# Performance work log

Hardware: AMD Instinct MI355X
Metric: run time of the kernel (lower is better)

## Reference

```python
import jax, jax.numpy as jnp
import numpy as np

HIDDEN = 2048
NUM_HEADS = 16
HEAD_DIM = HIDDEN // NUM_HEADS  # 128
ROPE_BASE = 10000.0


def setup_inputs() -> dict:
    key = jax.random.key(0)
    ks = jax.random.split(key, 5)
    B, T, C = 2, 2048, HIDDEN
    scale = 1.0 / np.sqrt(C)
    x = jax.random.normal(ks[0], (B, T, C), dtype=jnp.float32)
    Wq = jax.random.normal(ks[1], (C, C), dtype=jnp.float32) * scale
    Wk = jax.random.normal(ks[2], (C, C), dtype=jnp.float32) * scale
    Wv = jax.random.normal(ks[3], (C, C), dtype=jnp.float32) * scale
    Wo = jax.random.normal(ks[4], (C, C), dtype=jnp.float32) * scale
    return {"x": x, "Wq": Wq, "Wk": Wk, "Wv": Wv, "Wo": Wo}


def _rope_cos_sin(T, dtype):
    # inv_freq: [D/2]; emb: [T, D] = cat(freqs, freqs)
    inv_freq = 1.0 / (ROPE_BASE ** (jnp.arange(0, HEAD_DIM, 2, dtype=jnp.float32) / HEAD_DIM))
    t = jnp.arange(T, dtype=jnp.float32)
    freqs = t[:, None] * inv_freq[None, :]          # [T, D/2]
    emb = jnp.concatenate([freqs, freqs], axis=-1)  # [T, D]
    # broadcast shape [1, T, 1, D] to match q/k [B, T, H, D]
    return jnp.cos(emb)[None, :, None, :].astype(dtype), jnp.sin(emb)[None, :, None, :].astype(dtype)


def _rotate_half(u):
    u1, u2 = jnp.split(u, 2, axis=-1)
    return jnp.concatenate([-u2, u1], axis=-1)


def reference(x, Wq, Wk, Wv, Wo):
    B, T, C = x.shape
    H, D = NUM_HEADS, HEAD_DIM
    # QKV projections (torch Linear: x @ W.T). Weights here stored as [C, C] so use x @ W.
    q = (x @ Wq).reshape(B, T, H, D)
    k = (x @ Wk).reshape(B, T, H, D)
    v = (x @ Wv).reshape(B, T, H, D)
    cos, sin = _rope_cos_sin(T, x.dtype)
    q = q * cos + _rotate_half(q) * sin
    k = k * cos + _rotate_half(k) * sin
    # causal SDPA: scores [B, H, T, T]
    scale = 1.0 / jnp.sqrt(jnp.asarray(D, dtype=x.dtype))
    scores = jnp.einsum('bqhd,bkhd->bhqk', q, k) * scale
    causal = jnp.tril(jnp.ones((T, T), dtype=bool))
    scores = jnp.where(causal[None, None, :, :], scores, jnp.asarray(-jnp.inf, dtype=scores.dtype))
    attn = jax.nn.softmax(scores, axis=-1)
    out = jnp.einsum('bhqk,bkhd->bqhd', attn, v).reshape(B, T, C)
    return out @ Wo
```

## Files before the change

kernel.cpp:

```cpp
#include <hip/hip_runtime.h>
#include <hip/hip_bf16.h>

#define C_DIM 2048
#define NHEAD 16
#define HD 128
#define BB 2
#define TT 2048
#define MM (BB * TT)
#define NQT 32
#define N3 (3 * C_DIM)

typedef short short4v __attribute__((ext_vector_type(4)));
typedef short short8v __attribute__((ext_vector_type(8)));
typedef __bf16 bf16x4 __attribute__((ext_vector_type(4)));
typedef __bf16 bf16x8 __attribute__((ext_vector_type(8)));
typedef float f32x4 __attribute__((ext_vector_type(4)));

#define AS1 __attribute__((address_space(1)))
#define AS3 __attribute__((address_space(3)))

#define VMCNT(n) asm volatile("s_waitcnt vmcnt(" #n ")" ::: "memory")

__device__ __forceinline__ void load_lds16(const void* g, void* l) {
  __builtin_amdgcn_global_load_lds((const AS1 void*)g, (AS3 void*)l, 16, 0, 0);
}

__device__ __forceinline__ short f2bf(float f) {
  union { float f; unsigned u; } v; v.f = f;
  unsigned u = v.u;
  u += 0x7FFFu + ((u >> 16) & 1u);
  return (short)(u >> 16);
}
__device__ __forceinline__ float bf2f(short s) {
  union { unsigned u; float f; } v;
  v.u = ((unsigned)(unsigned short)s) << 16;
  return v.f;
}

__device__ __forceinline__ float exp2_fast(float x) {
  float r;
  asm("v_exp_f32 %0, %1" : "=v"(r) : "v"(x));
  return r;
}

__global__ __launch_bounds__(256) void cvt_x(const float* __restrict__ in,
                                             short* __restrict__ out, int n4) {
  int i = blockIdx.x * 256 + threadIdx.x;
  int stride = gridDim.x * 256;
  for (int idx = i; idx < n4; idx += stride) {
    float4 f = ((const float4*)in)[idx];
    short4v o;
    o[0] = f2bf(f.x); o[1] = f2bf(f.y); o[2] = f2bf(f.z); o[3] = f2bf(f.w);
    ((short4v*)out)[idx] = o;
  }
}

__global__ __launch_bounds__(256) void cvt_w_all(const float* __restrict__ Wq,
                                                 const float* __restrict__ Wk,
                                                 const float* __restrict__ Wv,
                                                 const float* __restrict__ Wo,
                                                 short* __restrict__ Wt) {
  __shared__ float tile[32][33];
  int z = blockIdx.z;
  const float* W = z == 0 ? Wq : z == 1 ? Wk : z == 2 ? Wv : Wo;
  short* dst = Wt + (size_t)z * C_DIM * C_DIM;
  int bx = blockIdx.x;
  int by = blockIdx.y;
  int lx = threadIdx.x & 31;
  int ly = threadIdx.x >> 5;
#pragma unroll
  for (int j = 0; j < 4; ++j) {
    int r = by * 32 + ly + j * 8;
    tile[ly + j * 8][lx] = W[(size_t)r * C_DIM + bx * 32 + lx];
  }
  __syncthreads();
#pragma unroll
  for (int j = 0; j < 4; ++j) {
    int n = bx * 32 + ly + j * 8;
    dst[(size_t)n * C_DIM + by * 32 + lx] = f2bf(tile[lx][ly + j * 8]);
  }
}

__global__ __launch_bounds__(256) void rope_tab(float2* __restrict__ tab) {
  int idx = blockIdx.x * 256 + threadIdx.x;
  int t = idx >> 6, d = idx & 63;
  float inv = expf(-9.210340371976184f * (float)d * (1.0f / 64.0f));
  float a = (float)t * inv;
  tab[idx] = make_float2(cosf(a), sinf(a));
}

template <bool F32OUT>
__global__ __launch_bounds__(512, 4) void gemm8w(const short* __restrict__ A,
                                                 const short* __restrict__ Bt,
                                                 void* __restrict__ Cout,
                                                 int M, int N, int K, int NBN) {
  __shared__ short sA[2][128 * 64];
  __shared__ short sB[2][128 * 64];
  const int tid = threadIdx.x;
  const int lane = tid & 63;
  const int w = tid >> 6;
  const int wm = w >> 2, wn = w & 3;
  const int r = lane & 15, g = lane >> 4;

  const int wg = blockIdx.x;
  const int mb = wg / NBN, nb = wg % NBN;
  const int m0 = mb * 128, n0 = nb * 128;

  f32x4 acc[4][2] = {};

  auto stage = [&](int buf, int kt) {
#pragma unroll
    for (int j = 0; j < 2; ++j) {
      int p = j * 512 + tid;
      int row = p >> 3;
      int c16 = (p & 7) ^ (row & 7);
      load_lds16(A + (size_t)(m0 + row) * K + kt * 64 + c16 * 8,
                 &sA[buf][(j * 512 + w * 64) * 8]);
    }
#pragma unroll
    for (int j = 0; j < 2; ++j) {
      int p = j * 512 + tid;
      int row = p >> 3;
      int c16 = (p & 7) ^ (row & 7);
      load_lds16(Bt + (size_t)(n0 + row) * K + kt * 64 + c16 * 8,
                 &sB[buf][(j * 512 + w * 64) * 8]);
    }
  };

  auto compute = [&](int buf) {
#pragma unroll
    for (int kk = 0; kk < 2; ++kk) {
      bf16x8 af[4], bv[2];
#pragma unroll
      for (int m = 0; m < 4; ++m) {
        int row = wm * 64 + m * 16 + r;
        af[m] = *(const bf16x8*)((const char*)&sA[buf][0] + row * 128 +
                                 (((kk * 4 + g) ^ (row & 7)) << 4));
      }
#pragma unroll
      for (int n = 0; n < 2; ++n) {
        int row = wn * 32 + n * 16 + r;
        bv[n] = *(const bf16x8*)((const char*)&sB[buf][0] + row * 128 +
                                 (((kk * 4 + g) ^ (row & 7)) << 4));
      }
      __builtin_amdgcn_s_setprio(1);
#pragma unroll
      for (int m = 0; m < 4; ++m)
#pragma unroll
        for (int n = 0; n < 2; ++n)
          acc[m][n] = __builtin_amdgcn_mfma_f32_16x16x32_bf16(af[m], bv[n], acc[m][n], 0, 0, 0);
      __builtin_amdgcn_s_setprio(0);
    }
  };

  const int NT = K >> 6;
  stage(0, 0);
  stage(1, 1);
  VMCNT(4);
  __builtin_amdgcn_s_barrier();

  for (int t = 0; t < NT; ++t) {
    const int cur = t & 1;
    compute(cur);
    if (t + 1 < NT) {
      asm volatile("" ::: "memory");
      __builtin_amdgcn_s_barrier();
      if (t + 2 < NT) {
        stage(cur, t + 2);
        VMCNT(4);
      } else {
        VMCNT(0);
      }
      asm volatile("" ::: "memory");
      __builtin_amdgcn_s_barrier();
    }
  }

#pragma unroll
  for (int m = 0; m < 4; ++m)
#pragma unroll
    for (int n = 0; n < 2; ++n)
#pragma unroll
      for (int q = 0; q < 4; ++q) {
        int row = m0 + wm * 64 + m * 16 + g * 4 + q;
        int col = n0 + wn * 32 + n * 16 + r;
        size_t off = (size_t)row * N + col;
        if constexpr (F32OUT) ((float*)Cout)[off] = acc[m][n][q];
        else ((short*)Cout)[off] = f2bf(acc[m][n][q]);
      }
}

__global__ __launch_bounds__(256) void rope_qk(const short* __restrict__ qkv,
                                               const float2* __restrict__ tab,
                                               short* __restrict__ Qr,
                                               short* __restrict__ Kr) {
  const short* src = qkv + (blockIdx.y ? C_DIM : 0);
  short* dst = blockIdx.y ? Kr : Qr;
  const float qs = blockIdx.y ? 1.0f : 0.12751744f;
  int rid = blockIdx.x * 4 + (threadIdx.x >> 6);
  int lane = threadIdx.x & 63;
  int t = rid & (TT - 1);
  int bh = rid >> 11;
  int b = bh >> 4, h = bh & 15;
  const short* in = src + ((size_t)(b * TT + t)) * N3 + h * HD;

  int v = *(const int*)(in + 2 * lane);
  int pv = __shfl_xor(v, 32, 64);
  float f0 = bf2f((short)(v & 0xFFFF)),  f1 = bf2f((short)(v >> 16));
  float p0 = bf2f((short)(pv & 0xFFFF)), p1 = bf2f((short)(pv >> 16));
  float4 cst = *(const float4*)(tab + (size_t)t * 64 + ((2 * lane) & 63));
  float s = (lane < 32) ? -1.0f : 1.0f;
  float o0 = (f0 * cst.x + s * p0 * cst.y) * qs;
  float o1 = (f1 * cst.z + s * p1 * cst.w) * qs;
  unsigned out2 = ((unsigned)(unsigned short)f2bf(o0)) |
                  (((unsigned)(unsigned short)f2bf(o1)) << 16);
  *(unsigned*)(dst + (size_t)rid * HD + 2 * lane) = out2;
}

__global__ __launch_bounds__(256) void v_tr(const short* __restrict__ qkv,
                                            short* __restrict__ Vt) {
  __shared__ short tl[64][132];
  int bh = blockIdx.y, b = bh >> 4, h = bh & 15;
  int t0 = blockIdx.x * 64;
  int tid = threadIdx.x;
  const short* vsrc = qkv + 2 * C_DIM;
#pragma unroll
  for (int i = 0; i < 4; ++i) {
    int c = i * 256 + tid;
    int row = c >> 4, cc = c & 15;
    short8v v = *(const short8v*)(vsrc + ((size_t)(b * TT + t0 + row)) * N3 + h * HD + cc * 8);
#pragma unroll
    for (int j = 0; j < 8; ++j) tl[row][cc * 8 + j] = v[j];
  }
  __syncthreads();
  int d = tid >> 1, half = tid & 1;
#pragma unroll
  for (int u = 0; u < 4; ++u) {
    short8v ov;
#pragma unroll
    for (int j = 0; j < 8; ++j) ov[j] = tl[half * 32 + u * 8 + j][d];
    *(short8v*)(Vt + ((size_t)bh * HD + d) * TT + t0 + half * 32 + u * 8) = ov;
  }
}

__global__ __launch_bounds__(256, 3) void attn_one(const short* __restrict__ Qr,
                                                   const short* __restrict__ Kr,
                                                   const short* __restrict__ Vt,
                                                   short* __restrict__ AO) {
  const int bx = blockIdx.x;
  const int j = bx >> 5, bh = bx & 31;
  const int qt = (j & 1) ? (j >> 1) : (NQT - 1 - (j >> 1));
  const int b = bh >> 4, h = bh & 15;
  const int tid = threadIdx.x;
  const int lane = tid & 63;
  const int w = tid >> 6;
  const int r = lane & 15, g = lane >> 4;

  __shared__ short sK[64 * 128];
  __shared__ short sV[128 * 64];
  __shared__ short sP[4][16 * 64];

  bf16x8 qf[4];
  {
    const short* qbp = Qr + ((size_t)bh * TT + qt * 64 + w * 16 + r) * HD + g * 8;
#pragma unroll
    for (int s = 0; s < 4; ++s) qf[s] = *(const bf16x8*)(qbp + s * 32);
  }

  f32x4 o[8] = {};
  float m = -1e30f, l = 0.f;

  short8v kreg[4], vreg[4];
  auto stage_load = [&](int kt) {
#pragma unroll
    for (int i = 0; i < 4; ++i) {
      int c = i * 256 + tid;
      kreg[i] = *(const short8v*)(Kr + ((size_t)bh * TT + kt * 64 + (c >> 4)) * HD + (c & 15) * 8);
    }
#pragma unroll
    for (int i = 0; i < 4; ++i) {
      int c = i * 256 + tid;
      vreg[i] = *(const short8v*)(Vt + ((size_t)bh * HD + (c >> 3)) * TT + kt * 64 + (c & 7) * 8);
    }
  };
  auto stage_write = [&]() {
#pragma unroll
    for (int i = 0; i < 4; ++i) {
      int c = i * 256 + tid;
      int row = c >> 4, cc = c & 15;
      int addr = (row * 256 + cc * 16) ^ ((row & 7) << 4);
      *(short8v*)((char*)sK + addr) = kreg[i];
    }
#pragma unroll
    for (int i = 0; i < 4; ++i) {
      int c = i * 256 + tid;
      int row = c >> 3, cc = c & 7;
      int addr = (row * 128 + cc * 16) ^ ((row & 7) << 4);
      *(short8v*)((char*)sV + addr) = vreg[i];
    }
  };

  char* pw = (char*)&sP[w][0];

  stage_load(0);
  stage_write();
  __syncthreads();

  for (int kt = 0; kt <= qt; ++kt) {
    f32x4 sacc[4] = {};
    __builtin_amdgcn_s_setprio(1);
#pragma unroll
    for (int nf = 0; nf < 4; ++nf) {
#pragma unroll
      for (int ss = 0; ss < 4; ++ss) {
        int krow = nf * 16 + r;
        int addr = (krow * 256 + (ss * 32 + g * 8) * 2) ^ ((krow & 7) << 4);
        bf16x8 kf = *(const bf16x8*)((char*)sK + addr);
        sacc[nf] = __builtin_amdgcn_mfma_f32_16x16x32_bf16(kf, qf[ss], sacc[nf], 0, 0, 0);
      }
    }
    __builtin_amdgcn_s_setprio(0);

    if (kt < qt) stage_load(kt + 1);

    if (kt == qt) {
#pragma unroll
      for (int nf = 0; nf < 4; ++nf)
#pragma unroll
        for (int q = 0; q < 4; ++q)
          if (nf * 16 + g * 4 + q > w * 16 + r) sacc[nf][q] = -1e30f;
    }

    float p01 = fmaxf(fmaxf(sacc[0][0], sacc[0][1]), fmaxf(sacc[0][2], sacc[0][3]));
    float p23 = fmaxf(fmaxf(sacc[1][0], sacc[1][1]), fmaxf(sacc[1][2], sacc[1][3]));
    float p45 = fmaxf(fmaxf(sacc[2][0], sacc[2][1]), fmaxf(sacc[2][2], sacc[2][3]));
    float p67 = fmaxf(fmaxf(sacc[3][0], sacc[3][1]), fmaxf(sacc[3][2], sacc[3][3]));
    float pmax = fmaxf(fmaxf(p01, p23), fmaxf(p45, p67));
    pmax = fmaxf(pmax, __shfl_xor(pmax, 16, 64));
    pmax = fmaxf(pmax, __shfl_xor(pmax, 32, 64));

    if (!__all(pmax - m <= 8.0f)) {
      float mnew = fmaxf(m, pmax);
      float alpha = exp2_fast(m - mnew);
      m = mnew;
      l *= alpha;
#pragma unroll
      for (int q = 0; q < 4; ++q) {
        float aq = __shfl(alpha, (g * 4 + q) | (lane & 48), 64);
#pragma unroll
        for (int nf2 = 0; nf2 < 8; ++nf2) o[nf2][q] *= aq;
      }
    }

    float s16 = 0.f;
#pragma unroll
    for (int nf = 0; nf < 4; ++nf) {
      f32x4 pe;
#pragma unroll
      for (int q = 0; q < 4; ++q) pe[q] = exp2_fast(sacc[nf][q] - m);
      s16 += (pe[0] + pe[1]) + (pe[2] + pe[3]);
      int addr = (r * 128 + nf * 32 + g * 8) ^ ((r & 7) << 4);
      *(bf16x4*)(pw + addr) = __builtin_convertvector(pe, bf16x4);
    }
    float rs = s16;
    rs += __shfl_xor(rs, 16, 64);
    rs += __shfl_xor(rs, 32, 64);
    l += rs;

    __builtin_amdgcn_s_setprio(1);
#pragma unroll
    for (int s2 = 0; s2 < 2; ++s2) {
      int paddr = (r * 128 + s2 * 64 + g * 16) ^ ((r & 7) << 4);
      bf16x8 pa = *(const bf16x8*)(pw + paddr);
#pragma unroll
      for (int nf2 = 0; nf2 < 8; ++nf2) {
        int drow = nf2 * 16 + r;
        int addr = (drow * 128 + (s2 * 32 + g * 8) * 2) ^ ((drow & 7) << 4);
        bf16x8 vb = *(const bf16x8*)((char*)sV + addr);
        o[nf2] = __builtin_amdgcn_mfma_f32_16x16x32_bf16(pa, vb, o[nf2], 0, 0, 0);
      }
    }
    __builtin_amdgcn_s_setprio(0);

    __syncthreads();
    if (kt < qt) {
      stage_write();
      __syncthreads();
    }
  }

  float linv = 1.0f / l;
  float lrow[4];
#pragma unroll
  for (int q = 0; q < 4; ++q)
    lrow[q] = __shfl(linv, (g * 4 + q) | (lane & 48), 64);
  short* ow = sK + w * 16 * 128;
#pragma unroll
  for (int nf2 = 0; nf2 < 8; ++nf2)
#pragma unroll
    for (int q = 0; q < 4; ++q)
      ow[(g * 4 + q) * 128 + nf2 * 16 + r] = f2bf(o[nf2][q] * lrow[q]);
  __syncthreads();

#pragma unroll
  for (int ch = 0; ch < 4; ++ch) {
    int c = ch * 256 + tid;
    int orow = c >> 4;
    int ocol = (c & 15) * 8;
    int t = qt * 64 + orow;
    *(short8v*)(AO + ((size_t)b * TT + t) * C_DIM + h * HD + ocol) =
        *(const short8v*)(sK + orow * 128 + ocol);
  }
}

extern "C" void kernel_launch(void* const* d_in, const int* in_sizes, int n_in,
                              void* d_out, int out_size, void* d_ws, size_t ws_size,
                              hipStream_t stream) {
  const float* x  = (const float*)d_in[0];
  const float* Wq = (const float*)d_in[1];
  const float* Wk = (const float*)d_in[2];
  const float* Wv = (const float*)d_in[3];
  const float* Wo = (const float*)d_in[4];

  char* ws = (char*)d_ws;
  size_t off = 0;
  auto take = [&](size_t bytes) {
    char* p = ws + off;
    off += (bytes + 255) & ~(size_t)255;
    return p;
  };
  const size_t xe = (size_t)MM * C_DIM;
  const size_t we = (size_t)C_DIM * C_DIM;
  short* xb   = (short*)take(xe * 2);
  short* wqkv = (short*)take(4 * we * 2);
  short* wot  = wqkv + 3 * we;
  short* qkv  = (short*)take(3 * xe * 2);
  short* Qr   = (short*)take(xe * 2);
  short* Kr   = (short*)take(xe * 2);
  short* Vtr  = (short*)take(xe * 2);
  float2* tab = (float2*)take((size_t)TT * 64 * sizeof(float2));
  short* AO   = qkv;

  cvt_x<<<2048, 256, 0, stream>>>(x, xb, (int)(xe / 4));
  cvt_w_all<<<dim3(64, 64, 4), 256, 0, stream>>>(Wq, Wk, Wv, Wo, wqkv);
  rope_tab<<<(TT * 64) / 256, 256, 0, stream>>>(tab);

  gemm8w<false><<<1536, 512, 0, stream>>>(xb, wqkv, qkv, MM, N3, C_DIM, N3 / 128);

  rope_qk<<<dim3(16384, 2), 256, 0, stream>>>(qkv, tab, Qr, Kr);
  v_tr<<<dim3(32, 32), 256, 0, stream>>>(qkv, Vtr);

  attn_one<<<1024, 256, 0, stream>>>(Qr, Kr, Vtr, AO);

  gemm8w<true><<<512, 512, 0, stream>>>(AO, wot, d_out, MM, C_DIM, C_DIM, C_DIM / 128);
}
```

Before: 289.4 us.

## Fuse RoPE and V transpose into QKV GEMM epilogue via LDS staging

The QKV projection GEMM now stages its 128x128 output tile in shared memory and writes Q and K directly with RoPE (and the Q scale) applied, and V directly in transposed layout. This removes the rope_qk and v_tr kernels and the round trip of the full bf16 qkv intermediate through global memory, along with two launches. In exchange the GEMM epilogue gets longer and does per-element table loads and LDS reads, which may add register pressure or bank conflicts in the epilogue.

```diff
diff --git a/kernel.cpp b/kernel.cpp
--- a/kernel.cpp
+++ b/kernel.cpp
@@ -89,13 +89,18 @@
   tab[idx] = make_float2(cosf(a), sinf(a));
 }
 
-template <bool F32OUT>
+template <int EPI>
 __global__ __launch_bounds__(512, 4) void gemm8w(const short* __restrict__ A,
                                                  const short* __restrict__ Bt,
                                                  void* __restrict__ Cout,
-                                                 int M, int N, int K, int NBN) {
-  __shared__ short sA[2][128 * 64];
-  __shared__ short sB[2][128 * 64];
+                                                 int M, int N, int K, int NBN,
+                                                 const float2* __restrict__ tab,
+                                                 short* __restrict__ Qr,
+                                                 short* __restrict__ Kr,
+                                                 short* __restrict__ Vt) {
+  __shared__ short smem[4 * 128 * 64];
+  short (*sA)[128 * 64] = (short(*)[128 * 64])smem;
+  short (*sB)[128 * 64] = (short(*)[128 * 64])(smem + 2 * 128 * 64);
   const int tid = threadIdx.x;
   const int lane = tid & 63;
   const int w = tid >> 6;
@@ -176,70 +181,72 @@
     }
   }
 
-#pragma unroll
-  for (int m = 0; m < 4; ++m)
-#pragma unroll
-    for (int n = 0; n < 2; ++n)
-#pragma unroll
-      for (int q = 0; q < 4; ++q) {
-        int row = m0 + wm * 64 + m * 16 + g * 4 + q;
-        int col = n0 + wn * 32 + n * 16 + r;
-        size_t off = (size_t)row * N + col;
-        if constexpr (F32OUT) ((float*)Cout)[off] = acc[m][n][q];
-        else ((short*)Cout)[off] = f2bf(acc[m][n][q]);
-      }
-}
-
-__global__ __launch_bounds__(256) void rope_qk(const short* __restrict__ qkv,
-                                               const float2* __restrict__ tab,
-                                               short* __restrict__ Qr,
-                                               short* __restrict__ Kr) {
-  const short* src = qkv + (blockIdx.y ? C_DIM : 0);
-  short* dst = blockIdx.y ? Kr : Qr;
-  const float qs = blockIdx.y ? 1.0f : 0.12751744f;
-  int rid = blockIdx.x * 4 + (threadIdx.x >> 6);
-  int lane = threadIdx.x & 63;
-  int t = rid & (TT - 1);
-  int bh = rid >> 11;
-  int b = bh >> 4, h = bh & 15;
-  const short* in = src + ((size_t)(b * TT + t)) * N3 + h * HD;
-
-  int v = *(const int*)(in + 2 * lane);
-  int pv = __shfl_xor(v, 32, 64);
-  float f0 = bf2f((short)(v & 0xFFFF)),  f1 = bf2f((short)(v >> 16));
-  float p0 = bf2f((short)(pv & 0xFFFF)), p1 = bf2f((short)(pv >> 16));
-  float4 cst = *(const float4*)(tab + (size_t)t * 64 + ((2 * lane) & 63));
-  float s = (lane < 32) ? -1.0f : 1.0f;
-  float o0 = (f0 * cst.x + s * p0 * cst.y) * qs;
-  float o1 = (f1 * cst.z + s * p1 * cst.w) * qs;
-  unsigned out2 = ((unsigned)(unsigned short)f2bf(o0)) |
-                  (((unsigned)(unsigned short)f2bf(o1)) << 16);
-  *(unsigned*)(dst + (size_t)rid * HD + 2 * lane) = out2;
-}
-
-__global__ __launch_bounds__(256) void v_tr(const short* __restrict__ qkv,
-                                            short* __restrict__ Vt) {
-  __shared__ short tl[64][132];
-  int bh = blockIdx.y, b = bh >> 4, h = bh & 15;
-  int t0 = blockIdx.x * 64;
-  int tid = threadIdx.x;
-  const short* vsrc = qkv + 2 * C_DIM;
-#pragma unroll
-  for (int i = 0; i < 4; ++i) {
-    int c = i * 256 + tid;
-    int row = c >> 4, cc = c & 15;
-    short8v v = *(const short8v*)(vsrc + ((size_t)(b * TT + t0 + row)) * N3 + h * HD + cc * 8);
-#pragma unroll
-    for (int j = 0; j < 8; ++j) tl[row][cc * 8 + j] = v[j];
-  }
-  __syncthreads();
-  int d = tid >> 1, half = tid & 1;
-#pragma unroll
-  for (int u = 0; u < 4; ++u) {
-    short8v ov;
-#pragma unroll
-    for (int j = 0; j < 8; ++j) ov[j] = tl[half * 32 + u * 8 + j][d];
-    *(short8v*)(Vt + ((size_t)bh * HD + d) * TT + t0 + half * 32 + u * 8) = ov;
+  if constexpr (EPI == 1) {
+#pragma unroll
+    for (int m = 0; m < 4; ++m)
+#pragma unroll
+      for (int n = 0; n < 2; ++n)
+#pragma unroll
+        for (int q = 0; q < 4; ++q) {
+          int row = m0 + wm * 64 + m * 16 + g * 4 + q;
+          int col = n0 + wn * 32 + n * 16 + r;
+          ((float*)Cout)[(size_t)row * N + col] = acc[m][n][q];
+        }
+  } else {
+    __syncthreads();
+    short* S = smem;
+#pragma unroll
+    for (int m = 0; m < 4; ++m)
+#pragma unroll
+      for (int n = 0; n < 2; ++n)
+#pragma unroll
+        for (int q = 0; q < 4; ++q) {
+          int row = wm * 64 + m * 16 + g * 4 + q;
+          int col = wn * 32 + n * 16 + r;
+          S[row * 130 + col] = f2bf(acc[m][n][q]);
+        }
+    __syncthreads();
+
+    const int z = nb >> 4;
+    const int h = nb & 15;
+    const int b = m0 >> 11;
+    const int bh = b * NHEAD + h;
+    const int t_base = m0 & (TT - 1);
+
+    if (z < 2) {
+      short* dst = (z == 0) ? Qr : Kr;
+      const float qs = (z == 0) ? 0.12751744f : 1.0f;
+#pragma unroll
+      for (int i = 0; i < 4; ++i) {
+        int c = i * 512 + tid;
+        int row = c >> 4;
+        int d0 = (c & 15) * 8;
+        int t = t_base + row;
+        bool hi = d0 >= 64;
+        int dbase = d0 & 63;
+        short8v ov;
+#pragma unroll
+        for (int jj = 0; jj < 8; ++jj) {
+          float u  = bf2f(S[row * 130 + d0 + jj]);
+          float pu = bf2f(S[row * 130 + ((d0 + jj + 64) & 127)]);
+          float2 cs = tab[(size_t)t * 64 + dbase + jj];
+          float val = hi ? (u * cs.x + pu * cs.y) : (u * cs.x - pu * cs.y);
+          ov[jj] = f2bf(val * qs);
+        }
+        *(short8v*)(dst + ((size_t)bh * TT + t) * HD + d0) = ov;
+      }
+    } else {
+#pragma unroll
+      for (int i = 0; i < 4; ++i) {
+        int c = i * 512 + tid;
+        int d = c >> 4;
+        int tc = (c & 15) * 8;
+        short8v ov;
+#pragma unroll
+        for (int jj = 0; jj < 8; ++jj) ov[jj] = S[(tc + jj) * 130 + d];
+        *(short8v*)(Vt + ((size_t)bh * HD + d) * TT + t_base + tc) = ov;
+      }
+    }
   }
 }
 
@@ -434,23 +441,21 @@
   short* xb   = (short*)take(xe * 2);
   short* wqkv = (short*)take(4 * we * 2);
   short* wot  = wqkv + 3 * we;
-  short* qkv  = (short*)take(3 * xe * 2);
   short* Qr   = (short*)take(xe * 2);
   short* Kr   = (short*)take(xe * 2);
   short* Vtr  = (short*)take(xe * 2);
+  short* AO   = (short*)take(xe * 2);
   float2* tab = (float2*)take((size_t)TT * 64 * sizeof(float2));
-  short* AO   = qkv;
 
   cvt_x<<<2048, 256, 0, stream>>>(x, xb, (int)(xe / 4));
   cvt_w_all<<<dim3(64, 64, 4), 256, 0, stream>>>(Wq, Wk, Wv, Wo, wqkv);
   rope_tab<<<(TT * 64) / 256, 256, 0, stream>>>(tab);
 
-  gemm8w<false><<<1536, 512, 0, stream>>>(xb, wqkv, qkv, MM, N3, C_DIM, N3 / 128);
-
-  rope_qk<<<dim3(16384, 2), 256, 0, stream>>>(qkv, tab, Qr, Kr);
-  v_tr<<<dim3(32, 32), 256, 0, stream>>>(qkv, Vtr);
+  gemm8w<2><<<1536, 512, 0, stream>>>(xb, wqkv, nullptr, MM, N3, C_DIM, N3 / 128,
+                                      tab, Qr, Kr, Vtr);
 
   attn_one<<<1024, 256, 0, stream>>>(Qr, Kr, Vtr, AO);
 
-  gemm8w<true><<<512, 512, 0, stream>>>(AO, wot, d_out, MM, C_DIM, C_DIM, C_DIM / 128);
-}
+  gemm8w<1><<<512, 512, 0, stream>>>(AO, wot, d_out, MM, C_DIM, C_DIM, C_DIM / 128,
+                                     nullptr, nullptr, nullptr, nullptr);
+}
```

After: 264.5 us, median of 3. -8.6%, faster.
